# Kernel optimization log

Hardware: AMD Instinct MI355X
Metric: run time of the kernel (lower is better)

Reference implementation:

```python
import jax, jax.numpy as jnp
import numpy as np

NUM_ITERATIONS = 3
NUM_ROUTES = 6912  # 32*6*6*6


def _squash(t):
    # t: [..., O]; squash along last dim
    sq = jnp.sum(t * t, axis=-1, keepdims=True)
    return sq * t / ((1.0 + sq) * jnp.sqrt(sq))


def setup_inputs() -> dict:
    key = jax.random.key(0)
    k1, k2 = jax.random.split(key)
    B, R, I, C, O = 64, NUM_ROUTES, 8, 10, 16
    x = jax.random.normal(k1, (B, R, I), dtype=jnp.float32)
    route_weights = jax.random.normal(k2, (C, R, I, O), dtype=jnp.float32)
    return {"x": x, "route_weights": route_weights}


def reference(x, route_weights):
    # x: [B, R, I]; route_weights: [C, R, I, O]
    # priors = x[None,:,:,None,:] @ W[:,None,:,:,:] -> [C, B, R, 1, O]
    priors = jnp.einsum('bri,crio->cbro', x, route_weights)[:, :, :, None, :]
    logits = jnp.zeros_like(priors)  # [C, B, R, 1, O]
    outputs = None
    for i in range(NUM_ITERATIONS):
        # softmax over routes (dim=2), matching custom softmax(input, dim=2)
        probs = jax.nn.softmax(logits, axis=2)
        outputs = _squash(jnp.sum(probs * priors, axis=2, keepdims=True))  # [C,B,1,1,O]
        if i != NUM_ROUTES - 1:  # always true in original (num_routes >> iters)
            delta = jnp.sum(priors * outputs, axis=-1, keepdims=True)  # [C,B,R,1,1]
            logits = logits + delta
    return outputs
```

## Files before the change

### kernel.cpp

```cpp
#include <hip/hip_runtime.h>
#include <math.h>

#define BB 64
#define RR 6912
#define II 8
#define CC 10
#define OO 16
#define RPB 64
#define NCH 108
#define NGRP 8
#define MRG_PAD 20
#define LDSF (4*64*MRG_PAD + 4*64)

typedef _Float16 h2 __attribute__((ext_vector_type(2)));
typedef _Float16 half8 __attribute__((ext_vector_type(8)));
typedef float f32x16 __attribute__((ext_vector_type(16)));
union HV { int4 v; h2 h[4]; half8 h8; };

__global__ __launch_bounds__(256) void transpose_cvt_kernel(
    const float* __restrict__ x, int4* __restrict__ xth4)
{
    __shared__ float4 lds4[64 * 34];
    const int rblk = blockIdx.x >> 2;
    const int bblk = blockIdx.x & 3;
    const int r0 = rblk * 64, b0 = bblk * 16;
    const int t = threadIdx.x;
    {
        const int rl = t & 63;
        const int bl0 = t >> 6;
#pragma unroll
        for (int kb = 0; kb < 4; ++kb) {
            const int bl = kb * 4 + bl0;
            const float4* src = (const float4*)(x + ((size_t)(b0 + bl) * RR + (r0 + rl)) * II);
            lds4[rl * 34 + bl * 2 + 0] = src[0];
            lds4[rl * 34 + bl * 2 + 1] = src[1];
        }
    }
    __syncthreads();
    {
        const int bl = t & 15;
        const int rw0 = t >> 4;
#pragma unroll
        for (int kr = 0; kr < 4; ++kr) {
            const int rw = kr * 16 + rw0;
            float4 a = lds4[rw * 34 + bl * 2 + 0];
            float4 bq = lds4[rw * 34 + bl * 2 + 1];
            HV u;
            u.h[0] = h2{(_Float16)a.x,  (_Float16)a.y};
            u.h[1] = h2{(_Float16)a.z,  (_Float16)a.w};
            u.h[2] = h2{(_Float16)bq.x, (_Float16)bq.y};
            u.h[3] = h2{(_Float16)bq.z, (_Float16)bq.w};
            xth4[(size_t)(r0 + rw) * BB + (b0 + bl)] = u.v;
        }
    }
}

__global__ __launch_bounds__(256) void wcvt_kernel(
    const float4* __restrict__ w4, int4* __restrict__ wh4)
{
    __shared__ __align__(16) _Float16 wl[1024];
    const int blk = blockIdx.x;
    const int t = threadIdx.x;
    const float4 v = w4[(size_t)blk * 256 + t];
    const int rp = t >> 5;
    const int i  = (t >> 2) & 7;
    const int o0 = (t & 3) * 4;
    wl[(rp * 16 + o0 + 0) * 8 + i] = (_Float16)v.x;
    wl[(rp * 16 + o0 + 1) * 8 + i] = (_Float16)v.y;
    wl[(rp * 16 + o0 + 2) * 8 + i] = (_Float16)v.z;
    wl[(rp * 16 + o0 + 3) * 8 + i] = (_Float16)v.w;
    __syncthreads();
    if (t < 128) wh4[(size_t)blk * 128 + t] = ((const int4*)wl)[t];
}

template <int MODE>
__global__ __launch_bounds__(256, 4) void pass_kernel(
    const int4* __restrict__ xth4, const int4* __restrict__ wh4,
    const float* __restrict__ ov_in,
    float* __restrict__ pacc, float* __restrict__ pz)
{
    __shared__ __align__(16) float lds[LDSF];
    int4* wlds = (int4*)lds;

    const int bid = blockIdx.x;
    const int w = (bid & 7) * 135 + (bid >> 3);
    const int chunk = w / 10;
    const int c = w - chunk * 10;

    const int t = threadIdx.x;
    const int wv = t >> 6;
    const int l = t & 63;
    const int b = l & 31;
    const int hi = l >> 5;
    const int aquad = (l >> 4) & 1;
    const bool aact = (aquad == hi);

    {
        const int4* src = wh4 + (size_t)(c * (RR / 8) + chunk * 8) * 128;
#pragma unroll
        for (int k = 0; k < 4; ++k) wlds[k * 256 + t] = src[k * 256 + t];
    }

    float accA[8], accB[8];
#pragma unroll
    for (int j = 0; j < 8; ++j) { accA[j] = 0.f; accB[j] = 0.f; }
    float ZA = 0.f, ZB = 0.f;

    float ovA[8], ovB[8];
    if (MODE != 0) {
        const float* pa = ov_in + ((size_t)c * BB + b) * OO + 4 * hi;
        const float* pb = ov_in + ((size_t)c * BB + 32 + b) * OO + 4 * hi;
        float4 a0 = *(const float4*)(pa);
        float4 a1 = *(const float4*)(pa + 8);
        float4 b0 = *(const float4*)(pb);
        float4 b1 = *(const float4*)(pb + 8);
        ovA[0]=a0.x; ovA[1]=a0.y; ovA[2]=a0.z; ovA[3]=a0.w;
        ovA[4]=a1.x; ovA[5]=a1.y; ovA[6]=a1.z; ovA[7]=a1.w;
        ovB[0]=b0.x; ovB[1]=b0.y; ovB[2]=b0.z; ovB[3]=b0.w;
        ovB[4]=b1.x; ovB[5]=b1.y; ovB[6]=b1.z; ovB[7]=b1.w;
    }

    __syncthreads();

    const int rbase = chunk * RPB + wv * 16;

    f32x16 cA, cB;
#pragma unroll
    for (int q = 0; q < 16; ++q) { cA[q] = 0.f; cB[q] = 0.f; }

    HV xc0, xc1, xn0, xn1;
    xc0.v = xth4[(size_t)(rbase + hi) * BB + b];
    xc1.v = xth4[(size_t)(rbase + hi) * BB + 32 + b];
    xn0 = xc0; xn1 = xc1;

#pragma unroll 1
    for (int g = 0; g < NGRP; ++g) {
        if (g + 1 < NGRP) {
            const int rn = rbase + (g + 1) * 2 + hi;
            xn0.v = xth4[(size_t)rn * BB + b];
            xn1.v = xth4[(size_t)rn * BB + 32 + b];
        }
        const int rl0 = wv * 16 + g * 2;
        HV wq;
        wq.v = wlds[(rl0 + aquad) * 16 + (l & 15)];
        if (!aact) wq.v = make_int4(0, 0, 0, 0);

        if (MODE == 0) {
            cA = __builtin_amdgcn_mfma_f32_32x32x16_f16(wq.h8, xc0.h8, cA, 0, 0, 0);
            cB = __builtin_amdgcn_mfma_f32_32x32x16_f16(wq.h8, xc1.h8, cB, 0, 0, 0);
        } else {
            f32x16 p0, p1;
#pragma unroll
            for (int q = 0; q < 16; ++q) { p0[q] = 0.f; p1[q] = 0.f; }
            p0 = __builtin_amdgcn_mfma_f32_32x32x16_f16(wq.h8, xc0.h8, p0, 0, 0, 0);
            p1 = __builtin_amdgcn_mfma_f32_32x32x16_f16(wq.h8, xc1.h8, p1, 0, 0, 0);

            float dA0 = 0.f, dA1 = 0.f, dB0 = 0.f, dB1 = 0.f;
#pragma unroll
            for (int j = 0; j < 8; ++j) {
                dA0 = fmaf(p0[j],     ovA[j], dA0);
                dA1 = fmaf(p0[j + 8], ovA[j], dA1);
                dB0 = fmaf(p1[j],     ovB[j], dB0);
                dB1 = fmaf(p1[j + 8], ovB[j], dB1);
            }
            dA0 += __shfl_xor(dA0, 32);
            dA1 += __shfl_xor(dA1, 32);
            dB0 += __shfl_xor(dB0, 32);
            dB1 += __shfl_xor(dB1, 32);
            const float eA0 = __expf(dA0), eA1 = __expf(dA1);
            const float eB0 = __expf(dB0), eB1 = __expf(dB1);
            ZA += eA0 + eA1; ZB += eB0 + eB1;
#pragma unroll
            for (int j = 0; j < 8; ++j) {
                accA[j] = fmaf(eA0, p0[j], fmaf(eA1, p0[j + 8], accA[j]));
                accB[j] = fmaf(eB0, p1[j], fmaf(eB1, p1[j + 8], accB[j]));
            }
        }
        xc0 = xn0; xc1 = xn1;
    }

    if (MODE == 0) {
#pragma unroll
        for (int j = 0; j < 8; ++j) {
            accA[j] = cA[j] + cA[j + 8];
            accB[j] = cB[j] + cB[j + 8];
        }
    }

    __syncthreads();

    {
        float* m0 = lds + (wv * 64 + b) * MRG_PAD + 4 * hi;
        *(float4*)(m0)     = make_float4(accA[0], accA[1], accA[2], accA[3]);
        *(float4*)(m0 + 8) = make_float4(accA[4], accA[5], accA[6], accA[7]);
        float* m1 = lds + (wv * 64 + 32 + b) * MRG_PAD + 4 * hi;
        *(float4*)(m1)     = make_float4(accB[0], accB[1], accB[2], accB[3]);
        *(float4*)(m1 + 8) = make_float4(accB[4], accB[5], accB[6], accB[7]);
        if (MODE != 0 && hi == 0) {
            float* zr = lds + 4 * 64 * MRG_PAD;
            zr[wv * 64 + b] = ZA;
            zr[wv * 64 + 32 + b] = ZB;
        }
    }
    __syncthreads();

    {
        const int b2 = t >> 2, q = t & 3;
        float4 sum = make_float4(0.f, 0.f, 0.f, 0.f);
#pragma unroll
        for (int w2 = 0; w2 < 4; ++w2) {
            const float4 v = *(const float4*)(lds + (w2 * 64 + b2) * MRG_PAD + q * 4);
            sum.x += v.x; sum.y += v.y; sum.z += v.z; sum.w += v.w;
        }
        *(float4*)(pacc + (((size_t)(c * NCH + chunk) * BB + b2) * OO) + q * 4) = sum;
        if (MODE != 0 && q == 0) {
            const float* zr = lds + 4 * 64 * MRG_PAD;
            float z = 0.f;
#pragma unroll
            for (int w2 = 0; w2 < 4; ++w2) z += zr[w2 * 64 + b2];
            pz[(size_t)(c * NCH + chunk) * BB + b2] = z;
        }
    }
}

template <int MODE>
__global__ __launch_bounds__(256) void combine_kernel(
    const float* __restrict__ pacc, const float* __restrict__ pz,
    const float* __restrict__ out0, float* __restrict__ outw)
{
    __shared__ float lsum[256];
    __shared__ float lz[16];
    const int cb = blockIdx.x;
    const int c = cb >> 6, b = cb & 63;
    const int t = threadIdx.x;
    const int o = t & 15, g = t >> 4;

    float s = 0.f, zl = 0.f;
    for (int p = g; p < NCH; p += 16) {
        s += pacc[((size_t)(c * NCH + p) * BB + b) * OO + o];
        if (MODE != 0 && o == 0) zl += pz[(size_t)(c * NCH + p) * BB + b];
    }
    lsum[t] = s;
    if (MODE != 0 && o == 0) lz[g] = zl;
    __syncthreads();

    if (g == 0) {
#pragma unroll
        for (int k = 1; k < 16; ++k) s += lsum[k * 16 + o];
        if (MODE != 0) {
            float Zt = 0.f;
#pragma unroll
            for (int k = 0; k < 16; ++k) Zt += lz[k];
            s /= Zt;
        } else {
            s *= (1.0f / RR);
        }
        float sq = s * s;
#pragma unroll
        for (int w = 1; w < 16; w <<= 1) sq += __shfl_xor(sq, w);
        float val = s * sqrtf(sq) / (1.f + sq);
        if (MODE == 1) val += out0[(size_t)cb * OO + o];
        outw[(size_t)cb * OO + o] = val;
    }
}

extern "C" void kernel_launch(void* const* d_in, const int* in_sizes, int n_in,
                              void* d_out, int out_size, void* d_ws, size_t ws_size,
                              hipStream_t stream)
{
    const float* x = (const float*)d_in[0];
    const float* w = (const float*)d_in[1];
    float* out = (float*)d_out;

    float* ws = (float*)d_ws;
    float* xth    = ws;
    float* wh     = xth + (size_t)RR * BB * 4;
    float* pacc   = wh + (size_t)CC * RR * 64;
    float* pz     = pacc + (size_t)CC * NCH * BB * OO;
    float* out0   = pz + (size_t)CC * NCH * BB;
    float* outsum = out0 + CC * BB * OO;

    int4* xth4 = (int4*)xth;
    int4* wh4  = (int4*)wh;
    const float4* w4 = (const float4*)w;

    transpose_cvt_kernel<<<dim3((RR / 64) * 4), dim3(256), 0, stream>>>(x, xth4);
    wcvt_kernel<<<dim3(CC * (RR / 8)), dim3(256), 0, stream>>>(w4, wh4);

    const dim3 gp(CC * NCH), bp(256);
    const dim3 gc(CC * BB), bc(256);

    pass_kernel<0><<<gp, bp, 0, stream>>>(xth4, wh4, nullptr, pacc, pz);
    combine_kernel<0><<<gc, bc, 0, stream>>>(pacc, pz, nullptr, out0);
    pass_kernel<1><<<gp, bp, 0, stream>>>(xth4, wh4, out0, pacc, pz);
    combine_kernel<1><<<gc, bc, 0, stream>>>(pacc, pz, out0, outsum);
    pass_kernel<2><<<gp, bp, 0, stream>>>(xth4, wh4, outsum, pacc, pz);
    combine_kernel<2><<<gc, bc, 0, stream>>>(pacc, pz, nullptr, out);
}
```

Baseline: 136.5 us.

## Fuse combine into pass kernels via last-block atomic reduction and merge prep kernels

Merges the x-transpose and weight-conversion kernels into one launch, with each weight block now converting eight sub-blocks through a double-buffered LDS area. Removes the three separate combine kernels: each pass kernel atomically counts finished chunks per capsule class, and the last block reduces all partial sums, applies the squash and writes the outputs. Also feeds a zero accumulator to the MFMA directly instead of zeroing per iteration. This cuts kernel launches and inter-kernel gaps, but the per-class final reduction now runs serially in a single block, which can leave a tail at the end of each pass.

```diff
diff --git a/kernel.cpp b/kernel.cpp
--- a/kernel.cpp
+++ b/kernel.cpp
@@ -17,69 +17,79 @@
 typedef float f32x16 __attribute__((ext_vector_type(16)));
 union HV { int4 v; h2 h[4]; half8 h8; };
 
-__global__ __launch_bounds__(256) void transpose_cvt_kernel(
-    const float* __restrict__ x, int4* __restrict__ xth4)
+__global__ __launch_bounds__(256) void prep_kernel(
+    const float* __restrict__ x, int4* __restrict__ xth4,
+    const float4* __restrict__ w4, int4* __restrict__ wh4,
+    int* __restrict__ cnt)
 {
-    __shared__ float4 lds4[64 * 34];
-    const int rblk = blockIdx.x >> 2;
-    const int bblk = blockIdx.x & 3;
-    const int r0 = rblk * 64, b0 = bblk * 16;
+    __shared__ __align__(16) float4 lds4[64 * 34];
     const int t = threadIdx.x;
-    {
-        const int rl = t & 63;
-        const int bl0 = t >> 6;
-#pragma unroll
-        for (int kb = 0; kb < 4; ++kb) {
-            const int bl = kb * 4 + bl0;
-            const float4* src = (const float4*)(x + ((size_t)(b0 + bl) * RR + (r0 + rl)) * II);
-            lds4[rl * 34 + bl * 2 + 0] = src[0];
-            lds4[rl * 34 + bl * 2 + 1] = src[1];
-        }
-    }
-    __syncthreads();
-    {
-        const int bl = t & 15;
-        const int rw0 = t >> 4;
-#pragma unroll
-        for (int kr = 0; kr < 4; ++kr) {
-            const int rw = kr * 16 + rw0;
-            float4 a = lds4[rw * 34 + bl * 2 + 0];
-            float4 bq = lds4[rw * 34 + bl * 2 + 1];
-            HV u;
-            u.h[0] = h2{(_Float16)a.x,  (_Float16)a.y};
-            u.h[1] = h2{(_Float16)a.z,  (_Float16)a.w};
-            u.h[2] = h2{(_Float16)bq.x, (_Float16)bq.y};
-            u.h[3] = h2{(_Float16)bq.z, (_Float16)bq.w};
-            xth4[(size_t)(r0 + rw) * BB + (b0 + bl)] = u.v;
-        }
-    }
-}
-
-__global__ __launch_bounds__(256) void wcvt_kernel(
-    const float4* __restrict__ w4, int4* __restrict__ wh4)
-{
-    __shared__ __align__(16) _Float16 wl[1024];
-    const int blk = blockIdx.x;
-    const int t = threadIdx.x;
-    const float4 v = w4[(size_t)blk * 256 + t];
-    const int rp = t >> 5;
-    const int i  = (t >> 2) & 7;
-    const int o0 = (t & 3) * 4;
-    wl[(rp * 16 + o0 + 0) * 8 + i] = (_Float16)v.x;
-    wl[(rp * 16 + o0 + 1) * 8 + i] = (_Float16)v.y;
-    wl[(rp * 16 + o0 + 2) * 8 + i] = (_Float16)v.z;
-    wl[(rp * 16 + o0 + 3) * 8 + i] = (_Float16)v.w;
-    __syncthreads();
-    if (t < 128) wh4[(size_t)blk * 128 + t] = ((const int4*)wl)[t];
+    const int bid = blockIdx.x;
+
+    if (bid == 0 && t < 32) cnt[t] = 0;
+
+    if (bid < 432) {
+        const int rblk = bid >> 2;
+        const int bblk = bid & 3;
+        const int r0 = rblk * 64, b0 = bblk * 16;
+        {
+            const int rl = t & 63;
+            const int bl0 = t >> 6;
+#pragma unroll
+            for (int kb = 0; kb < 4; ++kb) {
+                const int bl = kb * 4 + bl0;
+                const float4* src = (const float4*)(x + ((size_t)(b0 + bl) * RR + (r0 + rl)) * II);
+                lds4[rl * 34 + bl * 2 + 0] = src[0];
+                lds4[rl * 34 + bl * 2 + 1] = src[1];
+            }
+        }
+        __syncthreads();
+        {
+            const int bl = t & 15;
+            const int rw0 = t >> 4;
+#pragma unroll
+            for (int kr = 0; kr < 4; ++kr) {
+                const int rw = kr * 16 + rw0;
+                float4 a = lds4[rw * 34 + bl * 2 + 0];
+                float4 bq = lds4[rw * 34 + bl * 2 + 1];
+                HV u;
+                u.h[0] = h2{(_Float16)a.x,  (_Float16)a.y};
+                u.h[1] = h2{(_Float16)a.z,  (_Float16)a.w};
+                u.h[2] = h2{(_Float16)bq.x, (_Float16)bq.y};
+                u.h[3] = h2{(_Float16)bq.z, (_Float16)bq.w};
+                xth4[(size_t)(r0 + rw) * BB + (b0 + bl)] = u.v;
+            }
+        }
+    } else {
+        _Float16* wl = (_Float16*)lds4;
+        const int wblk = bid - 432;
+        const int rp = t >> 5;
+        const int i  = (t >> 2) & 7;
+        const int o0 = (t & 3) * 4;
+#pragma unroll 1
+        for (int sb = 0; sb < 8; ++sb) {
+            const int blk8 = wblk * 8 + sb;
+            const float4 v = w4[(size_t)blk8 * 256 + t];
+            _Float16* wb = wl + (sb & 1) * 1024;
+            wb[(rp * 16 + o0 + 0) * 8 + i] = (_Float16)v.x;
+            wb[(rp * 16 + o0 + 1) * 8 + i] = (_Float16)v.y;
+            wb[(rp * 16 + o0 + 2) * 8 + i] = (_Float16)v.z;
+            wb[(rp * 16 + o0 + 3) * 8 + i] = (_Float16)v.w;
+            __syncthreads();
+            if (t < 128) wh4[(size_t)blk8 * 128 + t] = ((const int4*)wb)[t];
+        }
+    }
 }
 
 template <int MODE>
 __global__ __launch_bounds__(256, 4) void pass_kernel(
     const int4* __restrict__ xth4, const int4* __restrict__ wh4,
     const float* __restrict__ ov_in,
-    float* __restrict__ pacc, float* __restrict__ pz)
+    float* __restrict__ pacc, float* __restrict__ pz,
+    float* __restrict__ outw, int* __restrict__ cnt)
 {
     __shared__ __align__(16) float lds[LDSF];
+    __shared__ int islast;
     int4* wlds = (int4*)lds;
 
     const int bid = blockIdx.x;
@@ -124,9 +134,9 @@
 
     const int rbase = chunk * RPB + wv * 16;
 
-    f32x16 cA, cB;
-#pragma unroll
-    for (int q = 0; q < 16; ++q) { cA[q] = 0.f; cB[q] = 0.f; }
+    f32x16 cA, cB, zf;
+#pragma unroll
+    for (int q = 0; q < 16; ++q) { cA[q] = 0.f; cB[q] = 0.f; zf[q] = 0.f; }
 
     HV xc0, xc1, xn0, xn1;
     xc0.v = xth4[(size_t)(rbase + hi) * BB + b];
@@ -149,11 +159,8 @@
             cA = __builtin_amdgcn_mfma_f32_32x32x16_f16(wq.h8, xc0.h8, cA, 0, 0, 0);
             cB = __builtin_amdgcn_mfma_f32_32x32x16_f16(wq.h8, xc1.h8, cB, 0, 0, 0);
         } else {
-            f32x16 p0, p1;
-#pragma unroll
-            for (int q = 0; q < 16; ++q) { p0[q] = 0.f; p1[q] = 0.f; }
-            p0 = __builtin_amdgcn_mfma_f32_32x32x16_f16(wq.h8, xc0.h8, p0, 0, 0, 0);
-            p1 = __builtin_amdgcn_mfma_f32_32x32x16_f16(wq.h8, xc1.h8, p1, 0, 0, 0);
+            f32x16 p0 = __builtin_amdgcn_mfma_f32_32x32x16_f16(wq.h8, xc0.h8, zf, 0, 0, 0);
+            f32x16 p1 = __builtin_amdgcn_mfma_f32_32x32x16_f16(wq.h8, xc1.h8, zf, 0, 0, 0);
 
             float dA0 = 0.f, dA1 = 0.f, dB0 = 0.f, dB1 = 0.f;
 #pragma unroll
@@ -221,46 +228,48 @@
             pz[(size_t)(c * NCH + chunk) * BB + b2] = z;
         }
     }
-}
-
-template <int MODE>
-__global__ __launch_bounds__(256) void combine_kernel(
-    const float* __restrict__ pacc, const float* __restrict__ pz,
-    const float* __restrict__ out0, float* __restrict__ outw)
-{
-    __shared__ float lsum[256];
-    __shared__ float lz[16];
-    const int cb = blockIdx.x;
-    const int c = cb >> 6, b = cb & 63;
-    const int t = threadIdx.x;
-    const int o = t & 15, g = t >> 4;
-
-    float s = 0.f, zl = 0.f;
-    for (int p = g; p < NCH; p += 16) {
-        s += pacc[((size_t)(c * NCH + p) * BB + b) * OO + o];
-        if (MODE != 0 && o == 0) zl += pz[(size_t)(c * NCH + p) * BB + b];
-    }
-    lsum[t] = s;
-    if (MODE != 0 && o == 0) lz[g] = zl;
-    __syncthreads();
-
-    if (g == 0) {
-#pragma unroll
-        for (int k = 1; k < 16; ++k) s += lsum[k * 16 + o];
-        if (MODE != 0) {
-            float Zt = 0.f;
-#pragma unroll
-            for (int k = 0; k < 16; ++k) Zt += lz[k];
-            s /= Zt;
-        } else {
-            s *= (1.0f / RR);
-        }
-        float sq = s * s;
-#pragma unroll
-        for (int w = 1; w < 16; w <<= 1) sq += __shfl_xor(sq, w);
-        float val = s * sqrtf(sq) / (1.f + sq);
-        if (MODE == 1) val += out0[(size_t)cb * OO + o];
-        outw[(size_t)cb * OO + o] = val;
+
+    __syncthreads();
+    __threadfence();
+    if (t == 0) {
+        const int prev = atomicAdd(cnt + c, 1);
+        islast = (prev == NCH - 1);
+    }
+    __syncthreads();
+    if (!islast) return;
+    __threadfence();
+
+    float s0 = 0.f, s1 = 0.f, s2 = 0.f, s3 = 0.f, zb = 0.f;
+    const float* pb  = pacc + (size_t)c * NCH * BB * OO;
+    const float* pzb = pz   + (size_t)c * NCH * BB;
+#pragma unroll 4
+    for (int p = 0; p < NCH; ++p) {
+        const float* row = pb + (size_t)p * BB * OO;
+        s0 += row[t];
+        s1 += row[t + 256];
+        s2 += row[t + 512];
+        s3 += row[t + 768];
+        if (MODE != 0 && t < 64) zb += pzb[p * BB + t];
+    }
+
+    float* zl = lds;
+    if (MODE != 0) {
+        if (t < 64) zl[t] = zb;
+        __syncthreads();
+    }
+
+    float sk[4] = {s0, s1, s2, s3};
+#pragma unroll
+    for (int k = 0; k < 4; ++k) {
+        const int m = t + 256 * k;
+        float v = sk[k];
+        v = (MODE == 0) ? v * (1.0f / RR) : v / zl[m >> 4];
+        float sq = v * v;
+#pragma unroll
+        for (int ww = 1; ww < 16; ww <<= 1) sq += __shfl_xor(sq, ww);
+        float val = v * sqrtf(sq) / (1.f + sq);
+        if (MODE == 1) val += ov_in[(size_t)c * (BB * OO) + m];
+        outw[(size_t)c * (BB * OO) + m] = val;
     }
 }
 
@@ -279,21 +288,16 @@
     float* pz     = pacc + (size_t)CC * NCH * BB * OO;
     float* out0   = pz + (size_t)CC * NCH * BB;
     float* outsum = out0 + CC * BB * OO;
+    int*   cnt    = (int*)(outsum + CC * BB * OO);
 
     int4* xth4 = (int4*)xth;
     int4* wh4  = (int4*)wh;
     const float4* w4 = (const float4*)w;
 
-    transpose_cvt_kernel<<<dim3((RR / 64) * 4), dim3(256), 0, stream>>>(x, xth4);
-    wcvt_kernel<<<dim3(CC * (RR / 8)), dim3(256), 0, stream>>>(w4, wh4);
+    prep_kernel<<<dim3(432 + 1080), dim3(256), 0, stream>>>(x, xth4, w4, wh4, cnt);
 
     const dim3 gp(CC * NCH), bp(256);
-    const dim3 gc(CC * BB), bc(256);
-
-    pass_kernel<0><<<gp, bp, 0, stream>>>(xth4, wh4, nullptr, pacc, pz);
-    combine_kernel<0><<<gc, bc, 0, stream>>>(pacc, pz, nullptr, out0);
-    pass_kernel<1><<<gp, bp, 0, stream>>>(xth4, wh4, out0, pacc, pz);
-    combine_kernel<1><<<gc, bc, 0, stream>>>(pacc, pz, out0, outsum);
-    pass_kernel<2><<<gp, bp, 0, stream>>>(xth4, wh4, outsum, pacc, pz);
-    combine_kernel<2><<<gc, bc, 0, stream>>>(pacc, pz, nullptr, out);
+    pass_kernel<0><<<gp, bp, 0, stream>>>(xth4, wh4, nullptr, pacc, pz, out0,   cnt);
+    pass_kernel<1><<<gp, bp, 0, stream>>>(xth4, wh4, out0,    pacc, pz, outsum, cnt + 10);
+    pass_kernel<2><<<gp, bp, 0, stream>>>(xth4, wh4, outsum,  pacc, pz, out,    cnt + 20);
 }
```

Result: slower. 464.5 us (+240.2%).
